# Kernel tuning notes

Hardware: AMD Instinct MI355X
Metric: run time of the kernel (lower is better)

The kernel has to match this reference:

```python
import jax, jax.numpy as jnp
import numpy as np

EPS = 1e-5  # torch GroupNorm default

def setup_inputs() -> dict:
    key = jax.random.key(0)
    k1, k2, k3, k4 = jax.random.split(key, 4)
    B = 1048576
    x = jax.random.uniform(k1, (B, 1, 1, 120), dtype=jnp.float32)  # [B,1,1,120]
    conv_w = jax.random.uniform(k2, (120, 1, 1, 120), dtype=jnp.float32, minval=-0.5, maxval=0.5)  # weight_org
    conv_b = jnp.zeros((120,), dtype=jnp.float32)
    gn_w = jnp.ones((120,), dtype=jnp.float32)
    gn_b = jnp.zeros((120,), dtype=jnp.float32)
    lin_w = jax.random.normal(k3, (1, 120), dtype=jnp.float32) * 0.1
    return {"x": x, "conv_w": conv_w, "conv_b": conv_b,
            "gn_w": gn_w, "gn_b": gn_b, "lin_w": lin_w}

def reference(x, conv_w, conv_b, gn_w, gn_b, lin_w):
    # Input binarize: sign(x - 0.5); weight binarize: sign(weight_org)
    xb = jnp.sign(x[:, 0, 0, :] - 0.5)        # [B,120], values in {-1,0,+1}
    wb = jnp.sign(conv_w[:, 0, 0, :])         # [120,120]
    # Conv2d with kernel (1,120) on [B,1,1,120] == GEMM; bias added after
    y = jnp.einsum('bk,ck->bc', xb, wb) + conv_b  # [B,120]
    # GroupNorm(1, 120): normalize over all 120 channels per sample
    mean = jnp.mean(y, axis=1, keepdims=True)
    var = jnp.var(y, axis=1, keepdims=True)
    y = (y - mean) * jax.lax.rsqrt(var + EPS) * gn_w + gn_b
    # Softsign
    y = y / (1.0 + jnp.abs(y))
    # BNNLinear forward: linear(input, weight) -- NO bias used
    out = y @ lin_w.T                          # [B,1]
    return out
```

## Files before the change

### kernel.cpp

```cpp
#include <hip/hip_runtime.h>

#define NCH 120

__global__ void prep_kernel(const float* __restrict__ conv_w,
                            const float* __restrict__ conv_b,
                            const float* __restrict__ gn_w,
                            const float* __restrict__ gn_b,
                            const float* __restrict__ lin_w,
                            unsigned* __restrict__ ws)
{
    __shared__ unsigned s_any;
    if (threadIdx.x == 0) s_any = 0u;
    __syncthreads();
    int c = threadIdx.x;
    if (c < NCH) {
        unsigned sw[4] = {0u,0u,0u,0u};
        unsigned nz[4] = {0u,0u,0u,0u};
        const float* wr = conv_w + c * NCH;
        for (int k = 0; k < NCH; ++k) {
            float w = wr[k];
            unsigned wd = (unsigned)k >> 5, bit = (unsigned)k & 31u;
            sw[wd] |= (w > 0.0f ? 1u : 0u) << bit;
            nz[wd] |= (w != 0.0f ? 1u : 0u) << bit;
        }
        bool anyz = !(nz[0] == 0xFFFFFFFFu && nz[1] == 0xFFFFFFFFu &&
                      nz[2] == 0xFFFFFFFFu && nz[3] == 0x00FFFFFFu);
        if (anyz) atomicOr(&s_any, 1u);
        for (int w = 0; w < 4; ++w) {
            ws[c * 4 + w]       = sw[w];
            ws[480 + c * 4 + w] = nz[w];
        }
        float* cf = (float*)(ws + 960);
        cf[c * 4 + 0] = conv_b[c] - 128.0f;
        cf[c * 4 + 1] = gn_w[c];
        cf[c * 4 + 2] = gn_b[c];
        cf[c * 4 + 3] = lin_w[c];
    }
    __syncthreads();
    if (threadIdx.x == 0) ws[1440] = s_any;
}

__global__ __launch_bounds__(256) void bnn_kernel(
    const float* __restrict__ x,
    const unsigned* __restrict__ ws,
    float* __restrict__ out,
    int B)
{
    __shared__ uint4  sh_sign[NCH];
    __shared__ uint4  sh_nz[NCH];
    __shared__ float4 sh_coef[NCH];
    __shared__ unsigned long long s_bal[4][121];
    __shared__ unsigned sh_flag;

    const int tid  = threadIdx.x;
    const int lane = tid & 63;
    const int wv   = tid >> 6;

    if (tid < NCH) {
        sh_sign[tid] = ((const uint4*)ws)[tid];
        sh_nz[tid]   = ((const uint4*)ws)[120 + tid];
        sh_coef[tid] = ((const float4*)ws)[240 + tid];
    }
    if (tid == 0) sh_flag = ws[1440];

    const long long wsample0 = (long long)blockIdx.x * 256 + wv * 64;
    const float* __restrict__ wx = x + wsample0 * NCH;
    unsigned minu = 0xFFFFFFFFu;
#pragma unroll
    for (int j = 0; j < 8; ++j) {
        float v[15];
#pragma unroll
        for (int k = 0; k < 15; ++k)
            v[k] = wx[(j * 15 + k) * 64 + lane];
#pragma unroll
        for (int k = 0; k < 15; ++k) {
            unsigned u = __float_as_uint(0.5f - v[k]);
            minu = min(minu, u);
            unsigned long long b = __ballot(v[k] > 0.5f);
            if (lane == 0) s_bal[wv][j * 15 + k] = b;
        }
    }
    const bool wave_slow = __any(minu == 0u);
    __syncthreads();

    const int bi = (int)wsample0 + lane;
    if (bi >= B) return;

    const unsigned bitpos = (unsigned)lane * 120u;
    const unsigned widx   = bitpos >> 5;
    const unsigned sh     = bitpos & 31u;
    const unsigned* wr = (const unsigned*)&s_bal[wv][0];
    unsigned t0 = wr[widx], t1 = wr[widx + 1], t2 = wr[widx + 2],
             t3 = wr[widx + 3], t4 = wr[widx + 4];
    unsigned sxa[4];
    sxa[0] = (unsigned)((((unsigned long long)t1 << 32) | t0) >> sh);
    sxa[1] = (unsigned)((((unsigned long long)t2 << 32) | t1) >> sh);
    sxa[2] = (unsigned)((((unsigned long long)t3 << 32) | t2) >> sh);
    sxa[3] = (unsigned)((((unsigned long long)t4 << 32) | t3) >> sh) & 0x00FFFFFFu;

    const bool fast = !wave_slow && (sh_flag == 0u);
    float acc = 0.0f;

    if (fast) {
        unsigned yw[30];
        unsigned sumY = 0u, sumYY = 0u;
#pragma unroll
        for (int c = 0; c < NCH; ++c) {
            uint4 w = sh_sign[c];
            unsigned p = __popc(~(sxa[0] ^ w.x));
            p = __popc(~(sxa[1] ^ w.y)) + p;
            p = __popc(~(sxa[2] ^ w.z)) + p;
            p = __popc(~(sxa[3] ^ w.w)) + p;
            unsigned Y = 2u * p - 8u;
            if ((c & 3) == 0) yw[c >> 2] = Y;
            else              yw[c >> 2] |= Y << ((c & 3) * 8);
            sumY  += Y;
            sumYY += __umul24(Y, Y);
        }
        float meanY = (float)sumY * (1.0f / 120.0f);
        float varY  = (float)sumYY * (1.0f / 120.0f) - meanY * meanY;
        float rstd  = __builtin_amdgcn_rsqf(varY + 1e-5f);
        float nb    = -(meanY - 128.0f) * rstd;
#pragma unroll
        for (int c = 0; c < NCH; ++c) {
            float4 cf = sh_coef[c];
            unsigned Y = (yw[c >> 2] >> ((c & 3) * 8)) & 0xFFu;
            float yf = (float)Y + cf.x;
            float n  = fmaf(yf, rstd, nb);
            float g  = fmaf(n, cf.y, cf.z);
            float s  = g * __builtin_amdgcn_rcpf(1.0f + fabsf(g));
            acc = fmaf(s, cf.w, acc);
        }
    } else {
        const float* __restrict__ xr = x + (long long)bi * NCH;
        unsigned nxa[4] = {0u,0u,0u,0u};
#pragma unroll
        for (int j = 0; j < 30; ++j) {
            float4 v = *(const float4*)(xr + 4 * j);
            unsigned u0 = __float_as_uint(0.5f - v.x);
            unsigned u1 = __float_as_uint(0.5f - v.y);
            unsigned u2 = __float_as_uint(0.5f - v.z);
            unsigned u3 = __float_as_uint(0.5f - v.w);
            const int w = j >> 3;
            const int p = (j & 7) * 4;
            nxa[w] |= (u0 != 0u ? 1u : 0u) << (p + 0);
            nxa[w] |= (u1 != 0u ? 1u : 0u) << (p + 1);
            nxa[w] |= (u2 != 0u ? 1u : 0u) << (p + 2);
            nxa[w] |= (u3 != 0u ? 1u : 0u) << (p + 3);
        }
        unsigned sumY = 0u, sumYY = 0u;
        for (int c = 0; c < NCH; ++c) {
            uint4 w = sh_sign[c];
            uint4 z = sh_nz[c];
            unsigned m0 = nxa[0] & z.x, m1 = nxa[1] & z.y;
            unsigned m2 = nxa[2] & z.z, m3 = nxa[3] & z.w;
            unsigned p = __popc((~(sxa[0] ^ w.x)) & m0)
                       + __popc((~(sxa[1] ^ w.y)) & m1)
                       + __popc((~(sxa[2] ^ w.z)) & m2)
                       + __popc((~(sxa[3] ^ w.w)) & m3);
            unsigned cnt = __popc(m0) + __popc(m1) + __popc(m2) + __popc(m3);
            int Y = 2 * (int)p - (int)cnt + 128;
            sumY  += (unsigned)Y;
            sumYY += (unsigned)(Y * Y);
        }
        float meanY = (float)sumY * (1.0f / 120.0f);
        float varY  = (float)sumYY * (1.0f / 120.0f) - meanY * meanY;
        float rstd  = __builtin_amdgcn_rsqf(varY + 1e-5f);
        float nb    = -(meanY - 128.0f) * rstd;
        for (int c = 0; c < NCH; ++c) {
            uint4 w = sh_sign[c];
            uint4 z = sh_nz[c];
            unsigned m0 = nxa[0] & z.x, m1 = nxa[1] & z.y;
            unsigned m2 = nxa[2] & z.z, m3 = nxa[3] & z.w;
            unsigned p = __popc((~(sxa[0] ^ w.x)) & m0)
                       + __popc((~(sxa[1] ^ w.y)) & m1)
                       + __popc((~(sxa[2] ^ w.z)) & m2)
                       + __popc((~(sxa[3] ^ w.w)) & m3);
            unsigned cnt = __popc(m0) + __popc(m1) + __popc(m2) + __popc(m3);
            int Y = 2 * (int)p - (int)cnt + 128;
            float4 cf = sh_coef[c];
            float yf = (float)Y + cf.x;
            float n  = fmaf(yf, rstd, nb);
            float g  = fmaf(n, cf.y, cf.z);
            float s  = g * __builtin_amdgcn_rcpf(1.0f + fabsf(g));
            acc = fmaf(s, cf.w, acc);
        }
    }
    out[bi] = acc;
}

extern "C" void kernel_launch(void* const* d_in, const int* in_sizes, int n_in,
                              void* d_out, int out_size, void* d_ws, size_t ws_size,
                              hipStream_t stream) {
    const float* x      = (const float*)d_in[0];
    const float* conv_w = (const float*)d_in[1];
    const float* conv_b = (const float*)d_in[2];
    const float* gn_w   = (const float*)d_in[3];
    const float* gn_b   = (const float*)d_in[4];
    const float* lin_w  = (const float*)d_in[5];
    unsigned* ws = (unsigned*)d_ws;
    float* out = (float*)d_out;

    const int B = in_sizes[0] / NCH;
    prep_kernel<<<1, 128, 0, stream>>>(conv_w, conv_b, gn_w, gn_b, lin_w, ws);
    const int grid = (B + 255) / 256;
    bnn_kernel<<<grid, 256, 0, stream>>>(x, ws, out, B);
}
```

Before: 139.0 us.

## Read weight bitmasks from global/scalar memory instead of LDS, pre-invert signs

```diff
diff --git a/kernel.cpp b/kernel.cpp
--- a/kernel.cpp
+++ b/kernel.cpp
@@ -27,7 +27,7 @@
                       nz[2] == 0xFFFFFFFFu && nz[3] == 0x00FFFFFFu);
         if (anyz) atomicOr(&s_any, 1u);
         for (int w = 0; w < 4; ++w) {
-            ws[c * 4 + w]       = sw[w];
+            ws[c * 4 + w]       = ~sw[w];
             ws[480 + c * 4 + w] = nz[w];
         }
         float* cf = (float*)(ws + 960);
@@ -38,6 +38,68 @@
     }
     __syncthreads();
     if (threadIdx.x == 0) ws[1440] = s_any;
+}
+
+__device__ float slow_sample(const float* __restrict__ xr,
+                             const unsigned* sxa,
+                             const unsigned* __restrict__ ws)
+{
+    const uint4*  nwp = (const uint4*)ws;
+    const uint4*  nzp = (const uint4*)(ws + 480);
+    const float4* cfp = (const float4*)(ws + 960);
+    unsigned nxa[4] = {0u,0u,0u,0u};
+    for (int j = 0; j < 30; ++j) {
+        float4 v = *(const float4*)(xr + 4 * j);
+        unsigned u0 = __float_as_uint(0.5f - v.x);
+        unsigned u1 = __float_as_uint(0.5f - v.y);
+        unsigned u2 = __float_as_uint(0.5f - v.z);
+        unsigned u3 = __float_as_uint(0.5f - v.w);
+        const int w = j >> 3;
+        const int p = (j & 7) * 4;
+        nxa[w] |= (u0 != 0u ? 1u : 0u) << (p + 0);
+        nxa[w] |= (u1 != 0u ? 1u : 0u) << (p + 1);
+        nxa[w] |= (u2 != 0u ? 1u : 0u) << (p + 2);
+        nxa[w] |= (u3 != 0u ? 1u : 0u) << (p + 3);
+    }
+    unsigned sumY = 0u, sumYY = 0u;
+    for (int c = 0; c < NCH; ++c) {
+        uint4 w = nwp[c];
+        uint4 z = nzp[c];
+        unsigned m0 = nxa[0] & z.x, m1 = nxa[1] & z.y;
+        unsigned m2 = nxa[2] & z.z, m3 = nxa[3] & z.w;
+        unsigned p = __popc((sxa[0] ^ w.x) & m0)
+                   + __popc((sxa[1] ^ w.y) & m1)
+                   + __popc((sxa[2] ^ w.z) & m2)
+                   + __popc((sxa[3] ^ w.w) & m3);
+        unsigned cnt = __popc(m0) + __popc(m1) + __popc(m2) + __popc(m3);
+        int Y = 2 * (int)p - (int)cnt + 128;
+        sumY  += (unsigned)Y;
+        sumYY += (unsigned)(Y * Y);
+    }
+    float meanY = (float)sumY * (1.0f / 120.0f);
+    float varY  = (float)sumYY * (1.0f / 120.0f) - meanY * meanY;
+    float rstd  = __builtin_amdgcn_rsqf(varY + 1e-5f);
+    float nb    = -(meanY - 128.0f) * rstd;
+    float acc = 0.0f;
+    for (int c = 0; c < NCH; ++c) {
+        uint4 w = nwp[c];
+        uint4 z = nzp[c];
+        unsigned m0 = nxa[0] & z.x, m1 = nxa[1] & z.y;
+        unsigned m2 = nxa[2] & z.z, m3 = nxa[3] & z.w;
+        unsigned p = __popc((sxa[0] ^ w.x) & m0)
+                   + __popc((sxa[1] ^ w.y) & m1)
+                   + __popc((sxa[2] ^ w.z) & m2)
+                   + __popc((sxa[3] ^ w.w) & m3);
+        unsigned cnt = __popc(m0) + __popc(m1) + __popc(m2) + __popc(m3);
+        int Y = 2 * (int)p - (int)cnt + 128;
+        float4 cf = cfp[c];
+        float yf = (float)Y + cf.x;
+        float n  = fmaf(yf, rstd, nb);
+        float g  = fmaf(n, cf.y, cf.z);
+        float s  = g * __builtin_amdgcn_rcpf(1.0f + fabsf(g));
+        acc = fmaf(s, cf.w, acc);
+    }
+    return acc;
 }
 
 __global__ __launch_bounds__(256) void bnn_kernel(
@@ -46,44 +108,49 @@
     float* __restrict__ out,
     int B)
 {
-    __shared__ uint4  sh_sign[NCH];
-    __shared__ uint4  sh_nz[NCH];
-    __shared__ float4 sh_coef[NCH];
     __shared__ unsigned long long s_bal[4][121];
-    __shared__ unsigned sh_flag;
 
     const int tid  = threadIdx.x;
     const int lane = tid & 63;
     const int wv   = tid >> 6;
 
-    if (tid < NCH) {
-        sh_sign[tid] = ((const uint4*)ws)[tid];
-        sh_nz[tid]   = ((const uint4*)ws)[120 + tid];
-        sh_coef[tid] = ((const float4*)ws)[240 + tid];
-    }
-    if (tid == 0) sh_flag = ws[1440];
+    const uint4*  nwp = (const uint4*)ws;
+    const float4* cfp = (const float4*)(ws + 960);
 
     const long long wsample0 = (long long)blockIdx.x * 256 + wv * 64;
     const float* __restrict__ wx = x + wsample0 * NCH;
     unsigned minu = 0xFFFFFFFFu;
-#pragma unroll
-    for (int j = 0; j < 8; ++j) {
-        float v[15];
-#pragma unroll
-        for (int k = 0; k < 15; ++k)
-            v[k] = wx[(j * 15 + k) * 64 + lane];
-#pragma unroll
-        for (int k = 0; k < 15; ++k) {
-            unsigned u = __float_as_uint(0.5f - v[k]);
+    const bool fullwave = (wsample0 + 64 <= (long long)B);
+    if (fullwave) {
+#pragma unroll
+        for (int j = 0; j < 8; ++j) {
+            float v[15];
+#pragma unroll
+            for (int k = 0; k < 15; ++k)
+                v[k] = wx[(j * 15 + k) * 64 + lane];
+#pragma unroll
+            for (int k = 0; k < 15; ++k) {
+                unsigned u = __float_as_uint(0.5f - v[k]);
+                minu = min(minu, u);
+                unsigned long long b = __ballot(v[k] > 0.5f);
+                if (lane == 0) s_bal[wv][j * 15 + k] = b;
+            }
+        }
+    } else {
+        const long long lim = (long long)B * NCH - wsample0 * NCH;
+        for (int it = 0; it < 120; ++it) {
+            long long idx = (long long)it * 64 + lane;
+            float vv = (idx < lim) ? wx[idx] : 0.0f;
+            unsigned u = __float_as_uint(0.5f - vv);
             minu = min(minu, u);
-            unsigned long long b = __ballot(v[k] > 0.5f);
-            if (lane == 0) s_bal[wv][j * 15 + k] = b;
+            unsigned long long b = __ballot(vv > 0.5f);
+            if (lane == 0) s_bal[wv][it] = b;
         }
     }
     const bool wave_slow = __any(minu == 0u);
     __syncthreads();
 
-    const int bi = (int)wsample0 + lane;
+    const long long bi = wsample0 + lane;
     if (bi >= B) return;
 
     const unsigned bitpos = (unsigned)lane * 120u;
@@ -98,19 +165,18 @@
     sxa[2] = (unsigned)((((unsigned long long)t3 << 32) | t2) >> sh);
     sxa[3] = (unsigned)((((unsigned long long)t4 << 32) | t3) >> sh) & 0x00FFFFFFu;
 
-    const bool fast = !wave_slow && (sh_flag == 0u);
-    float acc = 0.0f;
+    const bool fast = !wave_slow && (ws[1440] == 0u);
 
     if (fast) {
         unsigned yw[30];
         unsigned sumY = 0u, sumYY = 0u;
 #pragma unroll
         for (int c = 0; c < NCH; ++c) {
-            uint4 w = sh_sign[c];
-            unsigned p = __popc(~(sxa[0] ^ w.x));
-            p = __popc(~(sxa[1] ^ w.y)) + p;
-            p = __popc(~(sxa[2] ^ w.z)) + p;
-            p = __popc(~(sxa[3] ^ w.w)) + p;
+            uint4 w = nwp[c];
+            unsigned p = __popc(sxa[0] ^ w.x);
+            p = __popc(sxa[1] ^ w.y) + p;
+            p = __popc(sxa[2] ^ w.z) + p;
+            p = __popc(sxa[3] ^ w.w) + p;
             unsigned Y = 2u * p - 8u;
             if ((c & 3) == 0) yw[c >> 2] = Y;
             else              yw[c >> 2] |= Y << ((c & 3) * 8);
@@ -121,9 +187,10 @@
         float varY  = (float)sumYY * (1.0f / 120.0f) - meanY * meanY;
         float rstd  = __builtin_amdgcn_rsqf(varY + 1e-5f);
         float nb    = -(meanY - 128.0f) * rstd;
+        float acc = 0.0f;
 #pragma unroll
         for (int c = 0; c < NCH; ++c) {
-            float4 cf = sh_coef[c];
+            float4 cf = cfp[c];
             unsigned Y = (yw[c >> 2] >> ((c & 3) * 8)) & 0xFFu;
             float yf = (float)Y + cf.x;
             float n  = fmaf(yf, rstd, nb);
@@ -131,62 +198,10 @@
             float s  = g * __builtin_amdgcn_rcpf(1.0f + fabsf(g));
             acc = fmaf(s, cf.w, acc);
         }
+        out[bi] = acc;
     } else {
-        const float* __restrict__ xr = x + (long long)bi * NCH;
-        unsigned nxa[4] = {0u,0u,0u,0u};
-#pragma unroll
-        for (int j = 0; j < 30; ++j) {
-            float4 v = *(const float4*)(xr + 4 * j);
-            unsigned u0 = __float_as_uint(0.5f - v.x);
-            unsigned u1 = __float_as_uint(0.5f - v.y);
-            unsigned u2 = __float_as_uint(0.5f - v.z);
-            unsigned u3 = __float_as_uint(0.5f - v.w);
-            const int w = j >> 3;
-            const int p = (j & 7) * 4;
-            nxa[w] |= (u0 != 0u ? 1u : 0u) << (p + 0);
-            nxa[w] |= (u1 != 0u ? 1u : 0u) << (p + 1);
-            nxa[w] |= (u2 != 0u ? 1u : 0u) << (p + 2);
-            nxa[w] |= (u3 != 0u ? 1u : 0u) << (p + 3);
-        }
-        unsigned sumY = 0u, sumYY = 0u;
-        for (int c = 0; c < NCH; ++c) {
-            uint4 w = sh_sign[c];
-            uint4 z = sh_nz[c];
-            unsigned m0 = nxa[0] & z.x, m1 = nxa[1] & z.y;
-            unsigned m2 = nxa[2] & z.z, m3 = nxa[3] & z.w;
-            unsigned p = __popc((~(sxa[0] ^ w.x)) & m0)
-                       + __popc((~(sxa[1] ^ w.y)) & m1)
-                       + __popc((~(sxa[2] ^ w.z)) & m2)
-                       + __popc((~(sxa[3] ^ w.w)) & m3);
-            unsigned cnt = __popc(m0) + __popc(m1) + __popc(m2) + __popc(m3);
-            int Y = 2 * (int)p - (int)cnt + 128;
-            sumY  += (unsigned)Y;
-            sumYY += (unsigned)(Y * Y);
-        }
-        float meanY = (float)sumY * (1.0f / 120.0f);
-        float varY  = (float)sumYY * (1.0f / 120.0f) - meanY * meanY;
-        float rstd  = __builtin_amdgcn_rsqf(varY + 1e-5f);
-        float nb    = -(meanY - 128.0f) * rstd;
-        for (int c = 0; c < NCH; ++c) {
-            uint4 w = sh_sign[c];
-            uint4 z = sh_nz[c];
-            unsigned m0 = nxa[0] & z.x, m1 = nxa[1] & z.y;
-            unsigned m2 = nxa[2] & z.z, m3 = nxa[3] & z.w;
-            unsigned p = __popc((~(sxa[0] ^ w.x)) & m0)
-                       + __popc((~(sxa[1] ^ w.y)) & m1)
-                       + __popc((~(sxa[2] ^ w.z)) & m2)
-                       + __popc((~(sxa[3] ^ w.w)) & m3);
-            unsigned cnt = __popc(m0) + __popc(m1) + __popc(m2) + __popc(m3);
-            int Y = 2 * (int)p - (int)cnt + 128;
-            float4 cf = sh_coef[c];
-            float yf = (float)Y + cf.x;
-            float n  = fmaf(yf, rstd, nb);
-            float g  = fmaf(n, cf.y, cf.z);
-            float s  = g * __builtin_amdgcn_rcpf(1.0f + fabsf(g));
-            acc = fmaf(s, cf.w, acc);
-        }
-    }
-    out[bi] = acc;
+        out[bi] = slow_sample(x + bi * NCH, sxa, ws);
+    }
 }
 
 extern "C" void kernel_launch(void* const* d_in, const int* in_sizes, int n_in,
```

Result: slower. 151.9 us (+9.3%).
